# Kernel tuning notes

Hardware: AMD Instinct MI355X
Metric: run time of the kernel (lower is better)

Reference implementation:

```python
import jax, jax.numpy as jnp
import numpy as np

N_NODES = 100000
N_EDGES = 640000
D = 128
N_LAYERS = 4
N_GRAPHS = 512


def setup_inputs() -> dict:
    key = jax.random.key(0)
    ks = jax.random.split(key, 12)
    x = jax.random.normal(ks[0], (N_NODES, D), dtype=jnp.float32)
    edge_index = jax.random.randint(ks[1], (2, N_EDGES), 0, N_NODES, dtype=jnp.int64)
    batch = jnp.sort(jax.random.randint(ks[2], (N_NODES,), 0, N_GRAPHS, dtype=jnp.int64))
    s = 1.0 / np.sqrt(D)
    convW = jax.random.uniform(ks[3], (N_LAYERS, D, D), jnp.float32, -s, s)
    convB = jax.random.uniform(ks[4], (N_LAYERS, D), jnp.float32, -s, s)
    W1 = jax.random.uniform(ks[5], (D, D), jnp.float32, -s, s)
    b1 = jax.random.uniform(ks[6], (D,), jnp.float32, -s, s)
    W2 = jax.random.uniform(ks[7], (D, D), jnp.float32, -s, s)
    b2 = jax.random.uniform(ks[8], (D,), jnp.float32, -s, s)
    W3 = jax.random.uniform(ks[9], (D, 1), jnp.float32, -s, s)
    b3 = jax.random.uniform(ks[10], (1,), jnp.float32, -s, s)
    return {"x": x, "edge_index": edge_index, "batch": batch,
            "convW": convW, "convB": convB,
            "W1": W1, "b1": b1, "W2": W2, "b2": b2, "W3": W3, "b3": b3}


def reference(x, edge_index, batch, convW, convB, W1, b1, W2, b2, W3, b3):
    N = x.shape[0]
    # GCNConv default: add self-loops, symmetric deg^-1/2 normalization
    loops = jnp.arange(N, dtype=edge_index.dtype)
    src = jnp.concatenate([edge_index[0], loops])  # [E+N]
    dst = jnp.concatenate([edge_index[1], loops])
    deg = jax.ops.segment_sum(jnp.ones_like(dst, dtype=x.dtype), dst, num_segments=N)
    dinv = jnp.where(deg > 0, jax.lax.rsqrt(deg), 0.0)
    norm = (dinv[src] * dinv[dst])[:, None]  # [E+N, 1]
    h = x
    for i in range(N_LAYERS):
        hw = h @ convW[i]                                   # [N, D]
        msg = hw[src] * norm                                # gather + scale [E+N, D]
        agg = jax.ops.segment_sum(msg, dst, num_segments=N)  # scatter-add [N, D]
        h = jax.nn.relu(agg + convB[i])
    pooled = jax.ops.segment_sum(h, batch, num_segments=N_GRAPHS)  # [G, D]
    z = jax.nn.relu(pooled @ W1 + b1)
    z = jax.nn.relu(z @ W2 + b2)
    return jax.nn.sigmoid(z @ W3 + b3)  # [G, 1]
```

## Files before the change

kernel.cpp:

```cpp
#include <hip/hip_runtime.h>
#include <math.h>

#define D 128
#define LSTRIDE 136

typedef _Float16 half8 __attribute__((ext_vector_type(8)));
typedef _Float16 half4v __attribute__((ext_vector_type(4)));
typedef _Float16 half2v __attribute__((ext_vector_type(2)));
typedef float f32x4 __attribute__((ext_vector_type(4)));


__global__ void k_fat1(const int* __restrict__ ei, int* __restrict__ counts,
                       int* __restrict__ pidx, int E, int countBlocks,
                       const float* __restrict__ convW, _Float16* __restrict__ Wf) {
    if ((int)blockIdx.x < countBlocks) {
        int e0 = (blockIdx.x * blockDim.x + threadIdx.x) * 4;
        if (e0 + 3 < E) {
            int4 d4 = *(const int4*)(ei + E + e0);
            int4 p;
            p.x = atomicAdd(&counts[d4.x], 1);
            p.y = atomicAdd(&counts[d4.y], 1);
            p.z = atomicAdd(&counts[d4.z], 1);
            p.w = atomicAdd(&counts[d4.w], 1);
            *(int4*)(pidx + e0) = p;
        } else {
            for (int e = e0; e < E; e++) pidx[e] = atomicAdd(&counts[ei[E + e]], 1);
        }
    } else {
        const int bid = blockIdx.x - countBlocks;
        const int l = bid >> 3;
        const int slot = (bid & 7) * 256 + threadIdx.x;
        const float* W = convW + (size_t)l * D * D;
        const int p = slot >> 6, ln = slot & 63;
        const int s = p >> 3, c = p & 7;
        const int kbase = s * 32 + ((ln >> 4) << 3);
        const int n = (c << 4) + (ln & 15);
        half8 hv;
#pragma unroll
        for (int j = 0; j < 8; j++) hv[j] = (_Float16)W[(size_t)(kbase + j) * D + n];
        *(half8*)(Wf + (size_t)l * D * D + (size_t)slot * 8) = hv;
    }
}

__global__ __launch_bounds__(256) void k_scan1(const int* __restrict__ counts,
                                               int* __restrict__ rowptrP,
                                               int* __restrict__ rend,
                                               int* __restrict__ bsums,
                                               float* __restrict__ dinv, int N) {
    __shared__ int sh[256];
    const int t = threadIdx.x;
    const int base = blockIdx.x * 1024 + t * 4;
    int c[4], pj[4];
#pragma unroll
    for (int j = 0; j < 4; j++) {
        c[j] = (base + j < N) ? counts[base + j] : 0;
        pj[j] = (c[j] + 3) & ~3;
    }
#pragma unroll
    for (int j = 0; j < 4; j++)
        if (base + j < N) dinv[base + j] = rsqrtf((float)(c[j] + 1));
    int tsum = pj[0] + pj[1] + pj[2] + pj[3];
    sh[t] = tsum;
    __syncthreads();
    for (int off = 1; off < 256; off <<= 1) {
        int v = (t >= off) ? sh[t - off] : 0;
        __syncthreads();
        sh[t] += v;
        __syncthreads();
    }
    int run = (t == 0) ? 0 : sh[t - 1];
    if (t == 255) bsums[blockIdx.x] = sh[255];
#pragma unroll
    for (int j = 0; j < 4; j++) {
        if (base + j <= N) {
            rowptrP[base + j] = run;
            if (base + j < N) rend[base + j] = run + c[j];
        }
        run += pj[j];
    }
}


__global__ __launch_bounds__(256) void k_fat2(int* __restrict__ rowptrP,
                                              int* __restrict__ rend,
                                              const int* __restrict__ bsums,
                                              int NB, int N, int scanBlocks,
                                              const float* __restrict__ x,
                                              const float* __restrict__ dinv,
                                              _Float16* __restrict__ g16) {
    if ((int)blockIdx.x < scanBlocks) {
        __shared__ int pre[128];
        const int t = threadIdx.x;
        if (t < 128) pre[t] = (t < NB) ? bsums[t] : 0;
        __syncthreads();
        for (int off = 1; off < 128; off <<= 1) {
            int v = (t >= off && t < 128) ? pre[t - off] : 0;
            __syncthreads();
            if (t < 128) pre[t] += v;
            __syncthreads();
        }
        int i = blockIdx.x * blockDim.x + t;
        if (i <= N) {
            int b = i >> 10;
            int add = (b == 0) ? 0 : pre[b - 1];
            rowptrP[i] += add;
            if (i < N) rend[i] += add;
        }
    } else {
        int i = (blockIdx.x - scanBlocks) * blockDim.x + threadIdx.x;
        const int n8 = N * (D / 8);
        if (i >= n8) return;
        float s = dinv[i >> 4];
        const float4 v0 = *(const float4*)(x + (size_t)i * 8);
        const float4 v1 = *(const float4*)(x + (size_t)i * 8 + 4);
        half8 h;
        h[0] = (_Float16)(v0.x * s); h[1] = (_Float16)(v0.y * s);
        h[2] = (_Float16)(v0.z * s); h[3] = (_Float16)(v0.w * s);
        h[4] = (_Float16)(v1.x * s); h[5] = (_Float16)(v1.y * s);
        h[6] = (_Float16)(v1.z * s); h[7] = (_Float16)(v1.w * s);
        *(half8*)(g16 + (size_t)i * 8) = h;
    }
}

__global__ void k_fill(const int* __restrict__ ei, const int* __restrict__ rowptrP,
                       const int* __restrict__ pidx, int* __restrict__ srcs, int E) {
    int e0 = (blockIdx.x * blockDim.x + threadIdx.x) * 4;
    if (e0 + 3 < E) {
        int4 s4 = *(const int4*)(ei + e0);
        int4 d4 = *(const int4*)(ei + E + e0);
        int4 p4 = *(const int4*)(pidx + e0);
        int r0 = rowptrP[d4.x], r1 = rowptrP[d4.y], r2 = rowptrP[d4.z], r3 = rowptrP[d4.w];
        srcs[r0 + p4.x] = s4.x;
        srcs[r1 + p4.y] = s4.y;
        srcs[r2 + p4.z] = s4.z;
        srcs[r3 + p4.w] = s4.w;
    } else {
        for (int e = e0; e < E; e++)
            srcs[rowptrP[ei[E + e]] + pidx[e]] = ei[e];
    }
}


__global__ __launch_bounds__(512) void k_layer(
        const _Float16* __restrict__ gin,
        const int* __restrict__ rowptrP, const int* __restrict__ rend,
        const int* __restrict__ srcs,
        const float* __restrict__ dinv,
        const _Float16* __restrict__ Wf,
        const float* __restrict__ bias,
        _Float16* __restrict__ gout, int N, int last) {
    __shared__ _Float16 S[128 * LSTRIDE];

    const int tid  = threadIdx.x;
    const int w    = tid >> 6;
    const int lane = tid & 63;
    const int q    = lane >> 4;
    const int l16  = lane & 15;
    const int nb0  = blockIdx.x * 128;

    const int cb = l16 * 8;
    for (int it = 0; it < 4; ++it) {
        const int nl = w * 16 + q * 4 + it;
        const int node = nb0 + nl;
        float a[8];
#pragma unroll
        for (int j = 0; j < 8; j++) a[j] = 0.f;

        if (node < N) {
            half8 sv = *(const half8*)(gin + (size_t)node * D + cb);
#pragma unroll
            for (int j = 0; j < 8; j++) a[j] = (float)sv[j];
            int e = rowptrP[node];
            const int end = rend[node];
            for (; e + 3 < end; e += 4) {
                int4 s4 = *(const int4*)(srcs + e);
                half8 v0 = *(const half8*)(gin + (size_t)s4.x * D + cb);
                half8 v1 = *(const half8*)(gin + (size_t)s4.y * D + cb);
                half8 v2 = *(const half8*)(gin + (size_t)s4.z * D + cb);
                half8 v3 = *(const half8*)(gin + (size_t)s4.w * D + cb);
#pragma unroll
                for (int j = 0; j < 8; j++)
                    a[j] += ((float)v0[j] + (float)v1[j]) + ((float)v2[j] + (float)v3[j]);
            }
            for (; e < end; e++) {
                int s0 = srcs[e];
                half8 v0 = *(const half8*)(gin + (size_t)s0 * D + cb);
#pragma unroll
                for (int j = 0; j < 8; j++) a[j] += (float)v0[j];
            }
        }
        const float sc = (node < N) ? dinv[node] : 0.f;
        half8 o;
#pragma unroll
        for (int j = 0; j < 8; j++) o[j] = (_Float16)(a[j] * sc);
        *(half8*)(&S[nl * LSTRIDE + cb]) = o;
    }

    asm volatile("s_waitcnt lgkmcnt(0)" ::: "memory");

    f32x4 acc[8];
#pragma unroll
    for (int cc = 0; cc < 8; cc++) acc[cc] = (f32x4){0.f, 0.f, 0.f, 0.f};

    const int nl = w * 16 + l16;
#pragma unroll
    for (int s = 0; s < 4; s++) {
        half8 bf = *(const half8*)(&S[nl * LSTRIDE + s * 32 + q * 8]);
#pragma unroll
        for (int cc = 0; cc < 8; cc++) {
            half8 wh = *(const half8*)(Wf + (size_t)((s * 8 + cc) * 64 + lane) * 8);
            acc[cc] = __builtin_amdgcn_mfma_f32_16x16x32_f16(wh, bf, acc[cc], 0, 0, 0);
        }
    }

    const int node = nb0 + nl;
    if (node < N) {
        const float scale = last ? 1.0f : dinv[node];
        _Float16* rp = gout + (size_t)node * D + q * 4;
#pragma unroll
        for (int cc = 0; cc < 8; cc++) {
            const float4 bc = *(const float4*)(bias + cc * 16 + q * 4);
            half4v o;
            o[0] = (_Float16)(fmaxf(acc[cc][0] + bc.x, 0.f) * scale);
            o[1] = (_Float16)(fmaxf(acc[cc][1] + bc.y, 0.f) * scale);
            o[2] = (_Float16)(fmaxf(acc[cc][2] + bc.z, 0.f) * scale);
            o[3] = (_Float16)(fmaxf(acc[cc][3] + bc.w, 0.f) * scale);
            *(half4v*)(rp + cc * 16) = o;
        }
    }
}


__global__ __launch_bounds__(256) void k_poolhead(
        const _Float16* __restrict__ h, const int* __restrict__ batch,
        const float* __restrict__ W1, const float* __restrict__ b1,
        const float* __restrict__ W2, const float* __restrict__ b2,
        const float* __restrict__ W3, const float* __restrict__ b3,
        float* __restrict__ out, int N) {
    __shared__ int sb[2];
    __shared__ float part[4][D];
    __shared__ float v[D];
    __shared__ float z[D];
    __shared__ float red[D];

    const int g = blockIdx.x;
    const int t = threadIdx.x;

    if (t < 2) {
        int target = g + t;
        int lo = 0, hi = N;
        while (lo < hi) {
            int mid = (lo + hi) >> 1;
            if (batch[mid] < target) lo = mid + 1; else hi = mid;
        }
        sb[t] = lo;
    }
    __syncthreads();
    const int rs = sb[0], re = sb[1];

    const int w = t >> 6;
    const int lane = t & 63;
    const int c = lane * 2;

    float ax = 0.f, ay = 0.f;
    for (int r = rs + w; r < re; r += 4) {
        half2v vv = *(const half2v*)(h + (size_t)r * D + c);
        ax += (float)vv[0]; ay += (float)vv[1];
    }
    part[w][c] = ax;
    part[w][c + 1] = ay;
    __syncthreads();

    if (t < D) v[t] = part[0][t] + part[1][t] + part[2][t] + part[3][t];
    __syncthreads();

    if (t < D) {
        float s = b1[t];
        for (int k = 0; k < D; k++) s = fmaf(v[k], W1[(size_t)k * D + t], s);
        z[t] = fmaxf(s, 0.f);
    }
    __syncthreads();

    if (t < D) {
        float s = b2[t];
        for (int k = 0; k < D; k++) s = fmaf(z[k], W2[(size_t)k * D + t], s);
        red[t] = fmaxf(s, 0.f) * W3[t];
    }
    __syncthreads();
    for (int off = 64; off >= 1; off >>= 1) {
        if (t < off) red[t] += red[t + off];
        __syncthreads();
    }
    if (t == 0) out[g] = 1.f / (1.f + expf(-(red[0] + b3[0])));
}


extern "C" void kernel_launch(void* const* d_in, const int* in_sizes, int n_in,
                              void* d_out, int out_size, void* d_ws, size_t ws_size,
                              hipStream_t stream) {
    const float* x     = (const float*)d_in[0];
    const int*   ei    = (const int*)d_in[1];
    const int*   batch = (const int*)d_in[2];
    const float* convW = (const float*)d_in[3];
    const float* convB = (const float*)d_in[4];
    const float* W1 = (const float*)d_in[5];
    const float* b1 = (const float*)d_in[6];
    const float* W2 = (const float*)d_in[7];
    const float* b2 = (const float*)d_in[8];
    const float* W3 = (const float*)d_in[9];
    const float* b3 = (const float*)d_in[10];
    float* out = (float*)d_out;

    const int N = in_sizes[0] / D;
    const int E = in_sizes[1] / 2;
    const int G = out_size;
    const int NB = (N + 1023) / 1024;

    char* w = (char*)d_ws;
    size_t off = 0;
    auto alloc = [&](size_t bytes) -> char* {
        char* p = w + off;
        off += (bytes + 255) & ~(size_t)255;
        return p;
    };
    float*     dinv   = (float*)alloc((size_t)N * 4);
    _Float16*  gA     = (_Float16*)alloc((size_t)N * D * 2);
    _Float16*  gB     = (_Float16*)alloc((size_t)N * D * 2);
    _Float16*  Wf     = (_Float16*)alloc((size_t)4 * D * D * 2);
    int*       counts = (int*)alloc((size_t)N * 4);
    int*       rowptrP= (int*)alloc((size_t)(N + 1) * 4);
    int*       rend   = (int*)alloc((size_t)N * 4);
    int*       pidx   = (int*)alloc((size_t)E * 4);
    int*       srcs   = (int*)alloc((size_t)(E + 3 * N) * 4);
    int*       bsums  = (int*)alloc((size_t)NB * 4);

    hipMemsetAsync(counts, 0, (size_t)N * 4, stream);
    const int countBlocks = (E / 4 + 255) / 256;
    k_fat1<<<countBlocks + 32, 256, 0, stream>>>(ei, counts, pidx, E, countBlocks,
                                                 convW, Wf);
    k_scan1<<<NB, 256, 0, stream>>>(counts, rowptrP, rend, bsums, dinv, N);
    const int scanBlocks = (N + 1 + 255) / 256;
    const int cvtBlocks  = (N * (D / 8) + 255) / 256;
    k_fat2<<<scanBlocks + cvtBlocks, 256, 0, stream>>>(rowptrP, rend, bsums, NB, N,
                                                       scanBlocks, x, dinv, gA);
    k_fill<<<(E / 4 + 255) / 256, 256, 0, stream>>>(ei, rowptrP, pidx, srcs, E);

    const int layer_grid = (N + 127) / 128;
    const _Float16* gi = gA;
    _Float16* go = gB;
    for (int l = 0; l < 4; l++) {
        k_layer<<<layer_grid, 512, 0, stream>>>(gi, rowptrP, rend, srcs, dinv,
                                                Wf + (size_t)l * D * D,
                                                convB + (size_t)l * D,
                                                go, N, l == 3);
        const _Float16* tmp = go;
        go = (_Float16*)gi;
        gi = tmp;
    }

    k_poolhead<<<G, 256, 0, stream>>>(gi, batch, W1, b1, W2, b2, W3, b3, out, N);
}
```

Before: 358.6 us.

## Pad CSR rows to multiples of four with a zero node and interleave gathers

Each node's edge list is padded up to a multiple of four with a sentinel index pointing at an added all-zero row, so the aggregation loop has no scalar tail. Each thread now walks its four nodes' edge lists together, so many independent gathers are in flight at once. Blocks shrink to 256 threads and 64 nodes with a higher occupancy hint. The pooling kernel switches to 16-byte loads spread over 16 row groups. The padding costs some extra zero-row loads and assumes the prefix scan already reserved padded capacity in rowptr.

```diff
diff --git a/kernel.cpp b/kernel.cpp
--- a/kernel.cpp
+++ b/kernel.cpp
@@ -6,7 +6,6 @@
 
 typedef _Float16 half8 __attribute__((ext_vector_type(8)));
 typedef _Float16 half4v __attribute__((ext_vector_type(4)));
-typedef _Float16 half2v __attribute__((ext_vector_type(2)));
 typedef float f32x4 __attribute__((ext_vector_type(4)));
 
 
@@ -87,7 +86,9 @@
                                               int NB, int N, int scanBlocks,
                                               const float* __restrict__ x,
                                               const float* __restrict__ dinv,
-                                              _Float16* __restrict__ g16) {
+                                              _Float16* __restrict__ g16,
+                                              _Float16* __restrict__ g16b,
+                                              int* __restrict__ srcs) {
     if ((int)blockIdx.x < scanBlocks) {
         __shared__ int pre[128];
         const int t = threadIdx.x;
@@ -103,13 +104,28 @@
         if (i <= N) {
             int b = i >> 10;
             int add = (b == 0) ? 0 : pre[b - 1];
-            rowptrP[i] += add;
-            if (i < N) rend[i] += add;
+            int rp = rowptrP[i] + add;
+            rowptrP[i] = rp;
+            if (i < N) {
+                int re_ = rend[i] + add;
+                rend[i] = re_;
+                int pad = (-(re_ - rp)) & 3;
+                for (int k2 = 0; k2 < pad; k2++) srcs[re_ + k2] = N;
+            }
         }
     } else {
         int i = (blockIdx.x - scanBlocks) * blockDim.x + threadIdx.x;
         const int n8 = N * (D / 8);
-        if (i >= n8) return;
+        if (i >= n8) {
+            if (i < n8 + (D / 8)) {
+                half8 zz;
+#pragma unroll
+                for (int j = 0; j < 8; j++) zz[j] = (_Float16)0.f;
+                *(half8*)(g16 + (size_t)i * 8) = zz;
+                *(half8*)(g16b + (size_t)i * 8) = zz;
+            }
+            return;
+        }
         float s = dinv[i >> 4];
         const float4 v0 = *(const float4*)(x + (size_t)i * 8);
         const float4 v1 = *(const float4*)(x + (size_t)i * 8 + 4);
@@ -141,58 +157,79 @@
 }
 
 
-__global__ __launch_bounds__(512) void k_layer(
+__global__ __launch_bounds__(256, 4) void k_layer(
         const _Float16* __restrict__ gin,
-        const int* __restrict__ rowptrP, const int* __restrict__ rend,
+        const int* __restrict__ rowptrP,
         const int* __restrict__ srcs,
         const float* __restrict__ dinv,
         const _Float16* __restrict__ Wf,
         const float* __restrict__ bias,
         _Float16* __restrict__ gout, int N, int last) {
-    __shared__ _Float16 S[128 * LSTRIDE];
+    __shared__ _Float16 S[64 * LSTRIDE];
 
     const int tid  = threadIdx.x;
     const int w    = tid >> 6;
     const int lane = tid & 63;
     const int q    = lane >> 4;
     const int l16  = lane & 15;
-    const int nb0  = blockIdx.x * 128;
-
-    const int cb = l16 * 8;
-    for (int it = 0; it < 4; ++it) {
+    const int nb0  = blockIdx.x * 64;
+    const int cb   = l16 * 8;
+
+    int nd[4], bg[4], nc[4];
+    float sc[4];
+    float a[4][8];
+#pragma unroll
+    for (int it = 0; it < 4; it++) {
+        const int node = nb0 + w * 16 + q * 4 + it;
+        nd[it] = node;
+        const bool vv = node < N;
+        const int r0 = vv ? rowptrP[node] : 0;
+        const int r1 = vv ? rowptrP[node + 1] : 0;
+        bg[it] = r0;
+        nc[it] = (r1 - r0) >> 2;
+        sc[it] = vv ? dinv[node] : 0.f;
+    }
+#pragma unroll
+    for (int it = 0; it < 4; it++) {
+        if (nd[it] < N) {
+            half8 sv = *(const half8*)(gin + (size_t)nd[it] * D + cb);
+#pragma unroll
+            for (int j = 0; j < 8; j++) a[it][j] = (float)sv[j];
+        } else {
+#pragma unroll
+            for (int j = 0; j < 8; j++) a[it][j] = 0.f;
+        }
+    }
+
+    int mx = nc[0] > nc[1] ? nc[0] : nc[1];
+    mx = mx > nc[2] ? mx : nc[2];
+    mx = mx > nc[3] ? mx : nc[3];
+
+    for (int ch = 0; ch < mx; ch++) {
+        int4 s4[4];
+#pragma unroll
+        for (int it = 0; it < 4; it++)
+            if (ch < nc[it]) s4[it] = *(const int4*)(srcs + bg[it] + ch * 4);
+#pragma unroll
+        for (int it = 0; it < 4; it++) {
+            if (ch < nc[it]) {
+                half8 v0 = *(const half8*)(gin + (size_t)s4[it].x * D + cb);
+                half8 v1 = *(const half8*)(gin + (size_t)s4[it].y * D + cb);
+                half8 v2 = *(const half8*)(gin + (size_t)s4[it].z * D + cb);
+                half8 v3 = *(const half8*)(gin + (size_t)s4[it].w * D + cb);
+#pragma unroll
+                for (int j = 0; j < 8; j++)
+                    a[it][j] += ((float)v0[j] + (float)v1[j]) + ((float)v2[j] + (float)v3[j]);
+            }
+        }
+    }
+
+#pragma unroll
+    for (int it = 0; it < 4; it++) {
         const int nl = w * 16 + q * 4 + it;
-        const int node = nb0 + nl;
-        float a[8];
-#pragma unroll
-        for (int j = 0; j < 8; j++) a[j] = 0.f;
-
-        if (node < N) {
-            half8 sv = *(const half8*)(gin + (size_t)node * D + cb);
-#pragma unroll
-            for (int j = 0; j < 8; j++) a[j] = (float)sv[j];
-            int e = rowptrP[node];
-            const int end = rend[node];
-            for (; e + 3 < end; e += 4) {
-                int4 s4 = *(const int4*)(srcs + e);
-                half8 v0 = *(const half8*)(gin + (size_t)s4.x * D + cb);
-                half8 v1 = *(const half8*)(gin + (size_t)s4.y * D + cb);
-                half8 v2 = *(const half8*)(gin + (size_t)s4.z * D + cb);
-                half8 v3 = *(const half8*)(gin + (size_t)s4.w * D + cb);
-#pragma unroll
-                for (int j = 0; j < 8; j++)
-                    a[j] += ((float)v0[j] + (float)v1[j]) + ((float)v2[j] + (float)v3[j]);
-            }
-            for (; e < end; e++) {
-                int s0 = srcs[e];
-                half8 v0 = *(const half8*)(gin + (size_t)s0 * D + cb);
-#pragma unroll
-                for (int j = 0; j < 8; j++) a[j] += (float)v0[j];
-            }
-        }
-        const float sc = (node < N) ? dinv[node] : 0.f;
         half8 o;
 #pragma unroll
-        for (int j = 0; j < 8; j++) o[j] = (_Float16)(a[j] * sc);
+        for (int j = 0; j < 8; j++) o[j] = (_Float16)(a[it][j] * sc[it]);
         *(half8*)(&S[nl * LSTRIDE + cb]) = o;
     }
 
@@ -202,10 +239,10 @@
 #pragma unroll
     for (int cc = 0; cc < 8; cc++) acc[cc] = (f32x4){0.f, 0.f, 0.f, 0.f};
 
-    const int nl = w * 16 + l16;
+    const int nl2 = w * 16 + l16;
 #pragma unroll
     for (int s = 0; s < 4; s++) {
-        half8 bf = *(const half8*)(&S[nl * LSTRIDE + s * 32 + q * 8]);
+        half8 bf = *(const half8*)(&S[nl2 * LSTRIDE + s * 32 + q * 8]);
 #pragma unroll
         for (int cc = 0; cc < 8; cc++) {
             half8 wh = *(const half8*)(Wf + (size_t)((s * 8 + cc) * 64 + lane) * 8);
@@ -213,10 +250,10 @@
         }
     }
 
-    const int node = nb0 + nl;
-    if (node < N) {
-        const float scale = last ? 1.0f : dinv[node];
-        _Float16* rp = gout + (size_t)node * D + q * 4;
+    const int node2 = nb0 + nl2;
+    if (node2 < N) {
+        const float scale = last ? 1.0f : dinv[node2];
+        _Float16* rp = gout + (size_t)node2 * D + q * 4;
 #pragma unroll
         for (int cc = 0; cc < 8; cc++) {
             const float4 bc = *(const float4*)(bias + cc * 16 + q * 4);
@@ -238,8 +275,8 @@
         const float* __restrict__ W3, const float* __restrict__ b3,
         float* __restrict__ out, int N) {
     __shared__ int sb[2];
-    __shared__ float part[4][D];
-    __shared__ float v[D];
+    __shared__ float part[16][D];
+    __shared__ float pool[D];
     __shared__ float z[D];
     __shared__ float red[D];
 
@@ -260,23 +297,32 @@
 
     const int w = t >> 6;
     const int lane = t & 63;
-    const int c = lane * 2;
-
-    float ax = 0.f, ay = 0.f;
-    for (int r = rs + w; r < re; r += 4) {
-        half2v vv = *(const half2v*)(h + (size_t)r * D + c);
-        ax += (float)vv[0]; ay += (float)vv[1];
-    }
-    part[w][c] = ax;
-    part[w][c + 1] = ay;
-    __syncthreads();
-
-    if (t < D) v[t] = part[0][t] + part[1][t] + part[2][t] + part[3][t];
+    const int rw = w * 4 + (lane >> 4);
+    const int c8 = (lane & 15) * 8;
+
+    float ax[8];
+#pragma unroll
+    for (int j = 0; j < 8; j++) ax[j] = 0.f;
+    for (int r = rs + rw; r < re; r += 16) {
+        half8 vv = *(const half8*)(h + (size_t)r * D + c8);
+#pragma unroll
+        for (int j = 0; j < 8; j++) ax[j] += (float)vv[j];
+    }
+#pragma unroll
+    for (int j = 0; j < 8; j++) part[rw][c8 + j] = ax[j];
+    __syncthreads();
+
+    if (t < D) {
+        float s = 0.f;
+#pragma unroll
+        for (int gg = 0; gg < 16; gg++) s += part[gg][t];
+        pool[t] = s;
+    }
     __syncthreads();
 
     if (t < D) {
         float s = b1[t];
-        for (int k = 0; k < D; k++) s = fmaf(v[k], W1[(size_t)k * D + t], s);
+        for (int k = 0; k < D; k++) s = fmaf(pool[k], W1[(size_t)k * D + t], s);
         z[t] = fmaxf(s, 0.f);
     }
     __syncthreads();
@@ -324,8 +370,8 @@
         return p;
     };
     float*     dinv   = (float*)alloc((size_t)N * 4);
-    _Float16*  gA     = (_Float16*)alloc((size_t)N * D * 2);
-    _Float16*  gB     = (_Float16*)alloc((size_t)N * D * 2);
+    _Float16*  gA     = (_Float16*)alloc((size_t)(N + 1) * D * 2);
+    _Float16*  gB     = (_Float16*)alloc((size_t)(N + 1) * D * 2);
     _Float16*  Wf     = (_Float16*)alloc((size_t)4 * D * D * 2);
     int*       counts = (int*)alloc((size_t)N * 4);
     int*       rowptrP= (int*)alloc((size_t)(N + 1) * 4);
@@ -340,16 +386,17 @@
                                                  convW, Wf);
     k_scan1<<<NB, 256, 0, stream>>>(counts, rowptrP, rend, bsums, dinv, N);
     const int scanBlocks = (N + 1 + 255) / 256;
-    const int cvtBlocks  = (N * (D / 8) + 255) / 256;
+    const int cvtBlocks  = ((N + 1) * (D / 8) + 255) / 256;
     k_fat2<<<scanBlocks + cvtBlocks, 256, 0, stream>>>(rowptrP, rend, bsums, NB, N,
-                                                       scanBlocks, x, dinv, gA);
+                                                       scanBlocks, x, dinv, gA, gB,
+                                                       srcs);
     k_fill<<<(E / 4 + 255) / 256, 256, 0, stream>>>(ei, rowptrP, pidx, srcs, E);
 
-    const int layer_grid = (N + 127) / 128;
+    const int layer_grid = (N + 63) / 64;
     const _Float16* gi = gA;
     _Float16* go = gB;
     for (int l = 0; l < 4; l++) {
-        k_layer<<<layer_grid, 512, 0, stream>>>(gi, rowptrP, rend, srcs, dinv,
+        k_layer<<<layer_grid, 256, 0, stream>>>(gi, rowptrP, srcs, dinv,
                                                 Wf + (size_t)l * D * D,
                                                 convB + (size_t)l * D,
                                                 go, N, l == 3);
```

After: 366.7 us. 2.3% more time.

## Process nodes in degree-sorted order for load balance; widen pooling loads

Applied to the files above, without the earlier changes.

Builds a degree histogram during the scan and a counting-sort permutation that orders nodes by descending in-degree (capped at 63). The layer kernel then works on permuted node slots, so each wavefront handles nodes of similar degree, and its block shrinks to 64 nodes with 256 threads. This targets load imbalance in the gather loop. The cost is scattered row reads and writes in place of contiguous ones, plus extra setup work. The pooling kernel also switches to half8 loads spread over 16 row groups.

```diff
diff --git a/kernel.cpp b/kernel.cpp
--- a/kernel.cpp
+++ b/kernel.cpp
@@ -46,8 +46,10 @@
                                                int* __restrict__ rowptrP,
                                                int* __restrict__ rend,
                                                int* __restrict__ bsums,
-                                               float* __restrict__ dinv, int N) {
+                                               float* __restrict__ dinv,
+                                               int* __restrict__ degHist, int N) {
     __shared__ int sh[256];
+    __shared__ int lh[64];
     const int t = threadIdx.x;
     const int base = blockIdx.x * 1024 + t * 4;
     int c[4], pj[4];
@@ -59,6 +61,15 @@
 #pragma unroll
     for (int j = 0; j < 4; j++)
         if (base + j < N) dinv[base + j] = rsqrtf((float)(c[j] + 1));
+
+    if (t < 64) lh[t] = 0;
+    __syncthreads();
+#pragma unroll
+    for (int j = 0; j < 4; j++)
+        if (base + j < N) atomicAdd(&lh[c[j] < 63 ? c[j] : 63], 1);
+    __syncthreads();
+    if (t < 64 && lh[t]) atomicAdd(&degHist[t], lh[t]);
+
     int tsum = pj[0] + pj[1] + pj[2] + pj[3];
     sh[t] = tsum;
     __syncthreads();
@@ -123,50 +134,86 @@
 }
 
 __global__ void k_fill(const int* __restrict__ ei, const int* __restrict__ rowptrP,
-                       const int* __restrict__ pidx, int* __restrict__ srcs, int E) {
-    int e0 = (blockIdx.x * blockDim.x + threadIdx.x) * 4;
-    if (e0 + 3 < E) {
-        int4 s4 = *(const int4*)(ei + e0);
-        int4 d4 = *(const int4*)(ei + E + e0);
-        int4 p4 = *(const int4*)(pidx + e0);
-        int r0 = rowptrP[d4.x], r1 = rowptrP[d4.y], r2 = rowptrP[d4.z], r3 = rowptrP[d4.w];
-        srcs[r0 + p4.x] = s4.x;
-        srcs[r1 + p4.y] = s4.y;
-        srcs[r2 + p4.z] = s4.z;
-        srcs[r3 + p4.w] = s4.w;
+                       const int* __restrict__ pidx, int* __restrict__ srcs, int E,
+                       int fillBlocks, int N, const int* __restrict__ counts,
+                       const int* __restrict__ degHist, int* __restrict__ degCur,
+                       int* __restrict__ perm) {
+    if ((int)blockIdx.x < fillBlocks) {
+        int e0 = (blockIdx.x * blockDim.x + threadIdx.x) * 4;
+        if (e0 + 3 < E) {
+            int4 s4 = *(const int4*)(ei + e0);
+            int4 d4 = *(const int4*)(ei + E + e0);
+            int4 p4 = *(const int4*)(pidx + e0);
+            int r0 = rowptrP[d4.x], r1 = rowptrP[d4.y], r2 = rowptrP[d4.z], r3 = rowptrP[d4.w];
+            srcs[r0 + p4.x] = s4.x;
+            srcs[r1 + p4.y] = s4.y;
+            srcs[r2 + p4.z] = s4.z;
+            srcs[r3 + p4.w] = s4.w;
+        } else {
+            for (int e = e0; e < E; e++)
+                srcs[rowptrP[ei[E + e]] + pidx[e]] = ei[e];
+        }
     } else {
-        for (int e = e0; e < E; e++)
-            srcs[rowptrP[ei[E + e]] + pidx[e]] = ei[e];
-    }
-}
-
-
-__global__ __launch_bounds__(512) void k_layer(
+        __shared__ int lbase[64];
+        __shared__ int lh[64];
+        __shared__ int gb[64];
+        const int t = threadIdx.x;
+        const int i = ((int)blockIdx.x - fillBlocks) * blockDim.x + t;
+        if (t < 64) lh[t] = 0;
+        __syncthreads();
+        int deg = 0, lrank = 0;
+        const bool v = i < N;
+        if (v) {
+            int c = counts[i];
+            deg = c < 63 ? c : 63;
+            lrank = atomicAdd(&lh[deg], 1);
+        }
+        __syncthreads();
+        if (t < 64) gb[t] = lh[t] ? atomicAdd(&degCur[t], lh[t]) : 0;
+        if (t == 0) {
+            int run = 0;
+            for (int d = 63; d >= 0; d--) { lbase[d] = run; run += degHist[d]; }
+        }
+        __syncthreads();
+        if (v) perm[lbase[deg] + gb[deg] + lrank] = i;
+    }
+}
+
+
+__global__ __launch_bounds__(256) void k_layer(
         const _Float16* __restrict__ gin,
         const int* __restrict__ rowptrP, const int* __restrict__ rend,
         const int* __restrict__ srcs,
         const float* __restrict__ dinv,
+        const int* __restrict__ perm,
         const _Float16* __restrict__ Wf,
         const float* __restrict__ bias,
         _Float16* __restrict__ gout, int N, int last) {
-    __shared__ _Float16 S[128 * LSTRIDE];
+    __shared__ _Float16 S[64 * LSTRIDE];
 
     const int tid  = threadIdx.x;
     const int w    = tid >> 6;
     const int lane = tid & 63;
     const int q    = lane >> 4;
     const int l16  = lane & 15;
-    const int nb0  = blockIdx.x * 128;
-
-    const int cb = l16 * 8;
+    const int nb0  = blockIdx.x * 64;
+    const int cb   = l16 * 8;
+
+    int pn[4];
+#pragma unroll
+    for (int it = 0; it < 4; it++) {
+        const int slot = nb0 + w * 16 + q * 4 + it;
+        pn[it] = (slot < N) ? perm[slot] : -1;
+    }
+
     for (int it = 0; it < 4; ++it) {
         const int nl = w * 16 + q * 4 + it;
-        const int node = nb0 + nl;
+        const int node = pn[it];
         float a[8];
 #pragma unroll
         for (int j = 0; j < 8; j++) a[j] = 0.f;
 
-        if (node < N) {
+        if (node >= 0) {
             half8 sv = *(const half8*)(gin + (size_t)node * D + cb);
 #pragma unroll
             for (int j = 0; j < 8; j++) a[j] = (float)sv[j];
@@ -189,7 +236,7 @@
                 for (int j = 0; j < 8; j++) a[j] += (float)v0[j];
             }
         }
-        const float sc = (node < N) ? dinv[node] : 0.f;
+        const float sc = (node >= 0) ? dinv[node] : 0.f;
         half8 o;
 #pragma unroll
         for (int j = 0; j < 8; j++) o[j] = (_Float16)(a[j] * sc);
@@ -202,10 +249,10 @@
 #pragma unroll
     for (int cc = 0; cc < 8; cc++) acc[cc] = (f32x4){0.f, 0.f, 0.f, 0.f};
 
-    const int nl = w * 16 + l16;
+    const int nl2 = w * 16 + l16;
 #pragma unroll
     for (int s = 0; s < 4; s++) {
-        half8 bf = *(const half8*)(&S[nl * LSTRIDE + s * 32 + q * 8]);
+        half8 bf = *(const half8*)(&S[nl2 * LSTRIDE + s * 32 + q * 8]);
 #pragma unroll
         for (int cc = 0; cc < 8; cc++) {
             half8 wh = *(const half8*)(Wf + (size_t)((s * 8 + cc) * 64 + lane) * 8);
@@ -213,10 +260,11 @@
         }
     }
 
-    const int node = nb0 + nl;
-    if (node < N) {
-        const float scale = last ? 1.0f : dinv[node];
-        _Float16* rp = gout + (size_t)node * D + q * 4;
+    const int slot2 = nb0 + nl2;
+    const int node2 = (slot2 < N) ? perm[slot2] : -1;
+    if (node2 >= 0) {
+        const float scale = last ? 1.0f : dinv[node2];
+        _Float16* rp = gout + (size_t)node2 * D + q * 4;
 #pragma unroll
         for (int cc = 0; cc < 8; cc++) {
             const float4 bc = *(const float4*)(bias + cc * 16 + q * 4);
@@ -238,8 +286,8 @@
         const float* __restrict__ W3, const float* __restrict__ b3,
         float* __restrict__ out, int N) {
     __shared__ int sb[2];
-    __shared__ float part[4][D];
-    __shared__ float v[D];
+    __shared__ float part[16][D];
+    __shared__ float pool[D];
     __shared__ float z[D];
     __shared__ float red[D];
 
@@ -260,23 +308,32 @@
 
     const int w = t >> 6;
     const int lane = t & 63;
-    const int c = lane * 2;
-
-    float ax = 0.f, ay = 0.f;
-    for (int r = rs + w; r < re; r += 4) {
-        half2v vv = *(const half2v*)(h + (size_t)r * D + c);
-        ax += (float)vv[0]; ay += (float)vv[1];
-    }
-    part[w][c] = ax;
-    part[w][c + 1] = ay;
-    __syncthreads();
-
-    if (t < D) v[t] = part[0][t] + part[1][t] + part[2][t] + part[3][t];
+    const int rw = w * 4 + (lane >> 4);
+    const int c8 = (lane & 15) * 8;
+
+    float ax[8];
+#pragma unroll
+    for (int j = 0; j < 8; j++) ax[j] = 0.f;
+    for (int r = rs + rw; r < re; r += 16) {
+        half8 vv = *(const half8*)(h + (size_t)r * D + c8);
+#pragma unroll
+        for (int j = 0; j < 8; j++) ax[j] += (float)vv[j];
+    }
+#pragma unroll
+    for (int j = 0; j < 8; j++) part[rw][c8 + j] = ax[j];
+    __syncthreads();
+
+    if (t < D) {
+        float s = 0.f;
+#pragma unroll
+        for (int gg = 0; gg < 16; gg++) s += part[gg][t];
+        pool[t] = s;
+    }
     __syncthreads();
 
     if (t < D) {
         float s = b1[t];
-        for (int k = 0; k < D; k++) s = fmaf(v[k], W1[(size_t)k * D + t], s);
+        for (int k = 0; k < D; k++) s = fmaf(pool[k], W1[(size_t)k * D + t], s);
         z[t] = fmaxf(s, 0.f);
     }
     __syncthreads();
@@ -327,29 +384,36 @@
     _Float16*  gA     = (_Float16*)alloc((size_t)N * D * 2);
     _Float16*  gB     = (_Float16*)alloc((size_t)N * D * 2);
     _Float16*  Wf     = (_Float16*)alloc((size_t)4 * D * D * 2);
-    int*       counts = (int*)alloc((size_t)N * 4);
+    int*       counts = (int*)alloc((size_t)(N + 128) * 4);
+    int*       degHist= counts + N;
+    int*       degCur = counts + N + 64;
     int*       rowptrP= (int*)alloc((size_t)(N + 1) * 4);
     int*       rend   = (int*)alloc((size_t)N * 4);
     int*       pidx   = (int*)alloc((size_t)E * 4);
     int*       srcs   = (int*)alloc((size_t)(E + 3 * N) * 4);
     int*       bsums  = (int*)alloc((size_t)NB * 4);
-
-    hipMemsetAsync(counts, 0, (size_t)N * 4, stream);
+    int*       perm   = (int*)alloc((size_t)N * 4);
+
+    hipMemsetAsync(counts, 0, (size_t)(N + 128) * 4, stream);
     const int countBlocks = (E / 4 + 255) / 256;
     k_fat1<<<countBlocks + 32, 256, 0, stream>>>(ei, counts, pidx, E, countBlocks,
                                                  convW, Wf);
-    k_scan1<<<NB, 256, 0, stream>>>(counts, rowptrP, rend, bsums, dinv, N);
+    k_scan1<<<NB, 256, 0, stream>>>(counts, rowptrP, rend, bsums, dinv, degHist, N);
     const int scanBlocks = (N + 1 + 255) / 256;
     const int cvtBlocks  = (N * (D / 8) + 255) / 256;
     k_fat2<<<scanBlocks + cvtBlocks, 256, 0, stream>>>(rowptrP, rend, bsums, NB, N,
                                                        scanBlocks, x, dinv, gA);
-    k_fill<<<(E / 4 + 255) / 256, 256, 0, stream>>>(ei, rowptrP, pidx, srcs, E);
-
-    const int layer_grid = (N + 127) / 128;
+    const int fillBlocks = (E / 4 + 255) / 256;
+    const int rankBlocks = (N + 255) / 256;
+    k_fill<<<fillBlocks + rankBlocks, 256, 0, stream>>>(ei, rowptrP, pidx, srcs, E,
+                                                        fillBlocks, N, counts,
+                                                        degHist, degCur, perm);
+
+    const int layer_grid = (N + 63) / 64;
     const _Float16* gi = gA;
     _Float16* go = gB;
     for (int l = 0; l < 4; l++) {
-        k_layer<<<layer_grid, 512, 0, stream>>>(gi, rowptrP, rend, srcs, dinv,
+        k_layer<<<layer_grid, 256, 0, stream>>>(gi, rowptrP, rend, srcs, dinv, perm,
                                                 Wf + (size_t)l * D * D,
                                                 convB + (size_t)l * D,
                                                 go, N, l == 3);
```

Measured after the change: 357.3 us. Within noise of the previous version (-0.4%).
